# Optimization experiments

Hardware: AMD Instinct MI355X
Metric: run time of the kernel (lower is better)

The kernel has to match this reference:

```python
import jax, jax.numpy as jnp
import numpy as np

B, S, H, NH = 4, 2048, 2048, 16
HD = H // NH  # 128
CAUSAL = True


def setup_inputs() -> dict:
    key = jax.random.key(0)
    ks = jax.random.split(key, 5)
    mk = lambda k: jax.random.normal(k, (H, H), dtype=jnp.float32) * 0.02
    return {
        "x": jax.random.normal(ks[0], (B, S, H), dtype=jnp.float32),
        "w_q": mk(ks[1]),
        "w_k": mk(ks[2]),
        "w_v": mk(ks[3]),
        "w_o": mk(ks[4]),
    }


def reference(x, w_q, w_k, w_v, w_o):
    b, s, _ = x.shape
    # QKV projections (x @ W.T), split into heads: [b, nh, s, hd]
    q = (x @ w_q.T).reshape(b, s, NH, HD).transpose(0, 2, 1, 3)
    k = (x @ w_k.T).reshape(b, s, NH, HD).transpose(0, 2, 1, 3)
    v = (x @ w_v.T).reshape(b, s, NH, HD).transpose(0, 2, 1, 3)
    scale = 1.0 / jnp.sqrt(jnp.asarray(HD, dtype=x.dtype))
    score = jnp.einsum('bhqd,bhkd->bhqk', q, k) * scale  # [b, nh, s, s]
    if CAUSAL:
        mask = jnp.triu(jnp.ones((s, s), dtype=bool), k=1)
        score = jnp.where(mask, -jnp.inf, score)
    attn = jax.nn.softmax(score, axis=-1)
    o = jnp.einsum('bhqk,bhkd->bhqd', attn, v)  # [b, nh, s, hd]
    o = o.transpose(0, 2, 1, 3).reshape(b, s, H)
    return o @ w_o.T
```

## Files before the change

kernel.cpp:

```cpp
#include <hip/hip_runtime.h>

#define S_LEN 2048
#define HSZ   2048
#define M_TOK 8192

typedef float f32x4 __attribute__((ext_vector_type(4)));
typedef __bf16 bf16x8 __attribute__((ext_vector_type(8)));
typedef __bf16 bf16x4 __attribute__((ext_vector_type(4)));

typedef __attribute__((address_space(3))) __bf16 lds_bf16_t;
typedef __attribute__((address_space(1))) const __bf16 glb_bf16_t;

__device__ __forceinline__ void async16(__bf16* ldst, const __bf16* gsrc) {
    __builtin_amdgcn_global_load_lds((glb_bf16_t*)gsrc, (lds_bf16_t*)ldst, 16, 0, 0);
}

#define MFMA16(a, b, c) __builtin_amdgcn_mfma_f32_16x16x32_bf16((a), (b), (c), 0, 0, 0)

__global__ void cast_f32_bf16(const float* __restrict__ s, __bf16* __restrict__ d, int n4) {
    int idx = blockIdx.x * blockDim.x + threadIdx.x;
    int stride = gridDim.x * blockDim.x;
    for (int i = idx; i < n4; i += stride) {
        float4 v = ((const float4*)s)[i];
        bf16x4 o = { (__bf16)v.x, (__bf16)v.y, (__bf16)v.z, (__bf16)v.w };
        ((bf16x4*)d)[i] = o;
    }
}

__global__ void cast_weights(const float* __restrict__ wq, const float* __restrict__ wk,
                             const float* __restrict__ wv, const float* __restrict__ wo,
                             __bf16* __restrict__ wqkvb, __bf16* __restrict__ wob,
                             int n4seg) {
    int idx = blockIdx.x * blockDim.x + threadIdx.x;
    int stride = gridDim.x * blockDim.x;
    int total = 4 * n4seg;
    for (int i = idx; i < total; i += stride) {
        int seg = i / n4seg;
        int off = i - seg * n4seg;
        const float* s = (seg == 0) ? wq : (seg == 1) ? wk : (seg == 2) ? wv : wo;
        __bf16* d = (seg < 3) ? (wqkvb + (size_t)seg * n4seg * 4) : wob;
        float4 v = ((const float4*)s)[off];
        bf16x4 o = { (__bf16)v.x, (__bf16)v.y, (__bf16)v.z, (__bf16)v.w };
        ((bf16x4*)d)[off] = o;
    }
}


#define G_BAR() __builtin_amdgcn_s_barrier()
#define VMC(n)  do { asm volatile("s_waitcnt vmcnt(" #n ")" ::: "memory"); \
                     __builtin_amdgcn_sched_barrier(0); } while (0)

#define STAGE_A(bsel, kofs, half) do { \
    const __bf16* gp_ = A + (size_t)m0 * K + (kofs); \
    __bf16* sp_ = sm + (bsel) * 32768; \
    _Pragma("unroll") \
    for (int i_ = 0; i_ < 2; ++i_) { \
        int g_ = (w * 2 + i_) * 64 + lane; \
        int ri_ = g_ >> 3, c16_ = g_ & 7; \
        int row_ = (half) * 64 + (ri_ & 63) + (ri_ >> 6) * 128; \
        async16(&sp_[row_ * 64 + c16_ * 8], \
                &gp_[(size_t)row_ * K + ((c16_ ^ (row_ & 7)) * 8)]); \
    } } while (0)

#define STAGE_B(bsel, kofs, half) do { \
    const __bf16* gp_ = Bm + (size_t)n0 * K + (kofs); \
    __bf16* sp_ = sm + (bsel) * 32768 + 16384; \
    _Pragma("unroll") \
    for (int i_ = 0; i_ < 2; ++i_) { \
        int g_ = (w * 2 + i_) * 64 + lane; \
        int ri_ = g_ >> 3, c16_ = g_ & 7; \
        int row_ = (half) * 32 + (ri_ & 31) + (ri_ >> 5) * 64; \
        async16(&sp_[row_ * 64 + c16_ * 8], \
                &gp_[(size_t)row_ * K + ((c16_ ^ (row_ & 7)) * 8)]); \
    } } while (0)

#define LOAD_A(bsel, qm) do { \
    const __bf16* ap_ = sm + (bsel) * 32768; \
    _Pragma("unroll") \
    for (int mi_ = 0; mi_ < 4; ++mi_) { \
        int R_ = wm * 128 + (qm) * 64 + mi_ * 16 + l15; \
        int sw_ = (R_ & 7) << 3; \
        af[mi_][0] = *(const bf16x8*)&ap_[R_ * 64 + ((quad * 8) ^ sw_)]; \
        af[mi_][1] = *(const bf16x8*)&ap_[R_ * 64 + ((32 + quad * 8) ^ sw_)]; \
    } } while (0)

#define LOAD_B(bsel, qn, dst) do { \
    const __bf16* bp_ = sm + (bsel) * 32768 + 16384; \
    _Pragma("unroll") \
    for (int ni_ = 0; ni_ < 2; ++ni_) { \
        int R_ = wn * 64 + (qn) * 32 + ni_ * 16 + l15; \
        int sw_ = (R_ & 7) << 3; \
        dst[ni_][0] = *(const bf16x8*)&bp_[R_ * 64 + ((quad * 8) ^ sw_)]; \
        dst[ni_][1] = *(const bf16x8*)&bp_[R_ * 64 + ((32 + quad * 8) ^ sw_)]; \
    } } while (0)

#define MFMA_Q(qm, qn, bsrc) do { \
    __builtin_amdgcn_s_setprio(1); \
    _Pragma("unroll") \
    for (int mi_ = 0; mi_ < 4; ++mi_) \
        _Pragma("unroll") \
        for (int ni_ = 0; ni_ < 2; ++ni_) { \
            acc[(qm) * 4 + mi_][(qn) * 2 + ni_] = \
                MFMA16(af[mi_][0], bsrc[ni_][0], acc[(qm) * 4 + mi_][(qn) * 2 + ni_]); \
            acc[(qm) * 4 + mi_][(qn) * 2 + ni_] = \
                MFMA16(af[mi_][1], bsrc[ni_][1], acc[(qm) * 4 + mi_][(qn) * 2 + ni_]); \
        } \
    __builtin_amdgcn_s_setprio(0); \
} while (0)

#define GEMM256_MAIN() \
    constexpr int K = 2048; \
    const int w = threadIdx.x >> 6, lane = threadIdx.x & 63; \
    const int wm = w >> 2, wn = w & 3; \
    const int quad = lane >> 4, l15 = lane & 15; \
    const int m0 = blockIdx.y * 256, n0 = blockIdx.x * 256; \
    f32x4 acc[8][4] = {}; \
    bf16x8 af[4][2], b0f[2][2], b1f[2][2]; \
    const int NT = K >> 6; \
     \
     \
    STAGE_A(0, 0, 0); STAGE_B(0, 0, 0); STAGE_A(0, 0, 1); STAGE_B(0, 0, 1); \
    VMC(4); \
    G_BAR(); \
    LOAD_A(0, 0); \
    LOAD_B(0, 0, b0f); \
    _Pragma("unroll 2") \
    for (int kt = 0; kt < NT; ++kt) { \
        const int buf = kt & 1, nbuf = buf ^ 1; \
        const int k1 = (kt + 1) << 6; \
         \
        if (kt + 1 < NT) { STAGE_A(nbuf, k1, 0); VMC(2); } else { VMC(0); } \
        G_BAR(); \
        LOAD_B(buf, 1, b1f); \
        MFMA_Q(0, 0, b0f); \
         \
        if (kt + 1 < NT) STAGE_B(nbuf, k1, 0); \
        MFMA_Q(0, 1, b1f); \
        LOAD_A(buf, 1); \
        G_BAR(); \
         \
        if (kt + 1 < NT) { STAGE_A(nbuf, k1, 1); STAGE_B(nbuf, k1, 1); } \
        MFMA_Q(1, 1, b1f); \
        G_BAR(); \
         \
        MFMA_Q(1, 0, b0f); \
        if (kt + 1 < NT) { \
            VMC(4); \
            G_BAR(); \
            LOAD_A(nbuf, 0); \
            LOAD_B(nbuf, 0, b0f); \
        } \
    }

__global__ __launch_bounds__(512, 2) void gemm_qkv8(const __bf16* __restrict__ A,
                                                    const __bf16* __restrict__ Bm,
                                                    __bf16* __restrict__ Qo,
                                                    __bf16* __restrict__ Ko,
                                                    __bf16* __restrict__ VT) {
    __shared__ __bf16 sm[65536];
    GEMM256_MAIN();

    const int seg = n0 >> 11;
    const int nn  = (n0 & 2047) + wn * 64;
    if (seg < 2) {
        __bf16* Cv = seg ? Ko : Qo;
        #pragma unroll
        for (int mi = 0; mi < 8; ++mi)
            #pragma unroll
            for (int ni = 0; ni < 4; ++ni)
                #pragma unroll
                for (int i = 0; i < 4; ++i) {
                    int r = m0 + wm * 128 + mi * 16 + quad * 4 + i;
                    int c = nn + ni * 16 + l15;
                    Cv[(size_t)r * HSZ + c] = (__bf16)acc[mi][ni][i];
                }
    } else {
        #pragma unroll
        for (int mi = 0; mi < 8; ++mi)
            #pragma unroll
            for (int ni = 0; ni < 4; ++ni) {
                int r0 = m0 + wm * 128 + mi * 16 + quad * 4;
                int c  = nn + ni * 16 + l15;
                int bb = r0 >> 11, s = r0 & 2047;
                size_t base = ((size_t)(bb * 2048 + c) << 11) + s;
                bf16x4 v = { (__bf16)acc[mi][ni][0], (__bf16)acc[mi][ni][1],
                             (__bf16)acc[mi][ni][2], (__bf16)acc[mi][ni][3] };
                *(bf16x4*)&VT[base] = v;
            }
    }
}

__global__ __launch_bounds__(512, 2) void gemm_out(const __bf16* __restrict__ A,
                                                   const __bf16* __restrict__ Bm,
                                                   float* __restrict__ C) {
    __shared__ __bf16 sm[65536];
    GEMM256_MAIN();

    #pragma unroll
    for (int mi = 0; mi < 8; ++mi)
        #pragma unroll
        for (int ni = 0; ni < 4; ++ni)
            #pragma unroll
            for (int i = 0; i < 4; ++i) {
                int r = m0 + wm * 128 + mi * 16 + quad * 4 + i;
                int c = n0 + wn * 64 + ni * 16 + l15;
                C[(size_t)r * HSZ + c] = acc[mi][ni][i];
            }
}

__global__ __launch_bounds__(256, 2) void flash_fwd(const __bf16* __restrict__ Q,
                                                    const __bf16* __restrict__ K,
                                                    const __bf16* __restrict__ VT,
                                                    __bf16* __restrict__ O) {
    const int bx = blockIdx.x;
    const int qt = 15 - (bx >> 6);
    const int bh = bx & 63;
    const int q0 = qt * 128;

    const int tid  = threadIdx.x;
    const int w    = tid >> 6;
    const int lane = tid & 63;
    const int quad = lane >> 4;
    const int l15  = lane & 15;

    __shared__ __bf16 Ks[4 * 64 * 32];
    __shared__ __bf16 Vt[2 * 128 * 32];
    __shared__ __bf16 Ps[2 * 128 * 40];

    const int bq = bh >> 4, hh = bh & 15;
    const size_t base = ((size_t)bq * S_LEN) * HSZ + (size_t)hh * 128;
    const __bf16* Qg  = Q + base + (size_t)q0 * HSZ;
    const __bf16* VTg = VT + (size_t)bh * 128 * 2048;

    bf16x8 qf[2][4];
    #pragma unroll
    for (int mb = 0; mb < 2; ++mb)
        #pragma unroll
        for (int ks = 0; ks < 4; ++ks)
            qf[mb][ks] = *(const bf16x8*)&Qg[(size_t)(w * 32 + mb * 16 + l15) * HSZ + ks * 32 + quad * 8];

    f32x4 o_acc[2][8] = {};
    f32x4 psum[2] = {};

    const float scl = 0.08838834764831845f * 1.4426950408889634f;
    const float CC  = 8.0f * 1.4426950408889634f;
    bf16x8 ones;
    #pragma unroll
    for (int j = 0; j < 8; ++j) ones[j] = (__bf16)1.0f;

    const int n_kv = 2 * qt + 2;
    for (int kvt = 0; kvt < n_kv; ++kvt) {
        const int k0r = kvt * 64;
        __syncthreads();

        const __bf16* Kg = K + base + (size_t)k0r * HSZ;
        #pragma unroll
        for (int i = 0; i < 4; ++i) {
            int e  = (w * 4 + i) * 512 + lane * 8;
            int kc = e >> 11, r = (e >> 5) & 63, c = e & 31;
            async16(&Ks[e], &Kg[(size_t)r * HSZ + kc * 32 + c]);
        }
        #pragma unroll
        for (int i = 0; i < 4; ++i) {
            int e   = (w * 4 + i) * 512 + lane * 8;
            int kvc = e >> 12, dd = (e >> 5) & 127, c = e & 31;
            async16(&Vt[e], &VTg[(size_t)dd * 2048 + k0r + kvc * 32 + c]);
        }
        __syncthreads();

        f32x4 s_acc[2][4] = {};
        #pragma unroll
        for (int ks = 0; ks < 4; ++ks)
            #pragma unroll
            for (int nt = 0; nt < 4; ++nt) {
                bf16x8 bk = *(const bf16x8*)&Ks[ks * 2048 + (nt * 16 + l15) * 32 + quad * 8];
                s_acc[0][nt] = MFMA16(qf[0][ks], bk, s_acc[0][nt]);
                s_acc[1][nt] = MFMA16(qf[1][ks], bk, s_acc[1][nt]);
            }

        if (kvt >= 2 * qt) {
            #pragma unroll
            for (int mb = 0; mb < 2; ++mb) {
                int row = q0 + w * 32 + mb * 16 + quad * 4;
                #pragma unroll
                for (int nt = 0; nt < 4; ++nt) {
                    int col = k0r + nt * 16 + l15;
                    #pragma unroll
                    for (int i = 0; i < 4; ++i)
                        if (col > row + i) s_acc[mb][nt][i] = -1e30f;
                }
            }
        }

        #pragma unroll
        for (int mb = 0; mb < 2; ++mb)
            #pragma unroll
            for (int nt = 0; nt < 4; ++nt)
                #pragma unroll
                for (int i = 0; i < 4; ++i) {
                    float p = exp2f(s_acc[mb][nt][i] * scl - CC);
                    Ps[(nt >> 1) * 5120 + (w * 32 + mb * 16 + quad * 4 + i) * 40 + (nt & 1) * 16 + l15] = (__bf16)p;
                }

        #pragma unroll
        for (int ks2 = 0; ks2 < 2; ++ks2) {
            bf16x8 ap0 = *(const bf16x8*)&Ps[ks2 * 5120 + (w * 32 + l15) * 40 + quad * 8];
            bf16x8 ap1 = *(const bf16x8*)&Ps[ks2 * 5120 + (w * 32 + 16 + l15) * 40 + quad * 8];
            psum[0] = MFMA16(ap0, ones, psum[0]);
            psum[1] = MFMA16(ap1, ones, psum[1]);
            #pragma unroll
            for (int nt = 0; nt < 8; ++nt) {
                bf16x8 bv = *(const bf16x8*)&Vt[ks2 * 4096 + (nt * 16 + l15) * 32 + quad * 8];
                o_acc[0][nt] = MFMA16(ap0, bv, o_acc[0][nt]);
                o_acc[1][nt] = MFMA16(ap1, bv, o_acc[1][nt]);
            }
        }
    }

    __bf16* Og = O + base + (size_t)q0 * HSZ;
    #pragma unroll
    for (int mb = 0; mb < 2; ++mb)
        #pragma unroll
        for (int i = 0; i < 4; ++i) {
            float inv = 1.f / psum[mb][i];
            int r = w * 32 + mb * 16 + quad * 4 + i;
            #pragma unroll
            for (int nt = 0; nt < 8; ++nt)
                Og[(size_t)r * HSZ + nt * 16 + l15] = (__bf16)(o_acc[mb][nt][i] * inv);
        }
}

extern "C" void kernel_launch(void* const* d_in, const int* in_sizes, int n_in,
                              void* d_out, int out_size, void* d_ws, size_t ws_size,
                              hipStream_t stream) {
    const float* x  = (const float*)d_in[0];
    const float* wq = (const float*)d_in[1];
    const float* wk = (const float*)d_in[2];
    const float* wv = (const float*)d_in[3];
    const float* wo = (const float*)d_in[4];
    float* out = (float*)d_out;

    const size_t nX = (size_t)M_TOK * HSZ;
    const size_t nW = (size_t)HSZ * HSZ;

    char* ws = (char*)d_ws;
    __bf16* xb    = (__bf16*)ws;  ws += nX * 2;
    __bf16* wqkvb = (__bf16*)ws;  ws += 3 * nW * 2;
    __bf16* wob   = (__bf16*)ws;  ws += nW * 2;
    __bf16* Qb    = (__bf16*)ws;  ws += nX * 2;
    __bf16* Kb    = (__bf16*)ws;  ws += nX * 2;
    __bf16* VTb   = (__bf16*)ws;  ws += nX * 2;
    __bf16* Ob    = (__bf16*)ws;  ws += nX * 2;

    cast_f32_bf16<<<2048, 256, 0, stream>>>(x, xb, (int)(nX / 4));
    cast_weights<<<2048, 256, 0, stream>>>(wq, wk, wv, wo, wqkvb, wob, (int)(nW / 4));

    dim3 gq(3 * HSZ / 256, M_TOK / 256);
    gemm_qkv8<<<gq, 512, 0, stream>>>(xb, wqkvb, Qb, Kb, VTb);

    flash_fwd<<<64 * (S_LEN / 128), 256, 0, stream>>>(Qb, Kb, VTb, Ob);

    dim3 gg(HSZ / 256, M_TOK / 256);
    gemm_out<<<gg, 512, 0, stream>>>(Ob, wob, out);
}
```

Baseline: 509.9 us.

## Double-buffer K/V tiles in flash attention and prefetch the next tile

The flash attention kernel now keeps two LDS buffers for the K and V^T tiles. It issues async global-to-LDS loads for the next KV tile before computing on the current one, so each iteration needs one barrier instead of two and load latency can overlap with MFMA work. The P staging buffer shrinks to one 32-column chunk that is reused across two sub-steps, which offsets the larger K/V footprint. MFMA sections are wrapped in s_setprio raises. Total LDS use grows, which could limit how many blocks fit on a CU.

```diff
diff --git a/kernel.cpp b/kernel.cpp
--- a/kernel.cpp
+++ b/kernel.cpp
@@ -117,8 +117,6 @@
     f32x4 acc[8][4] = {}; \
     bf16x8 af[4][2], b0f[2][2], b1f[2][2]; \
     const int NT = K >> 6; \
-     \
-     \
     STAGE_A(0, 0, 0); STAGE_B(0, 0, 0); STAGE_A(0, 0, 1); STAGE_B(0, 0, 1); \
     VMC(4); \
     G_BAR(); \
@@ -208,6 +206,22 @@
             }
 }
 
+#define FSTAGE(b, kvt_) do { \
+    const int k0s_ = (kvt_) * 64; \
+    const __bf16* Kg_ = K + base + (size_t)k0s_ * HSZ; \
+    _Pragma("unroll") \
+    for (int i_ = 0; i_ < 4; ++i_) { \
+        int e_ = (w * 4 + i_) * 512 + lane * 8; \
+        int kc_ = e_ >> 11, r_ = (e_ >> 5) & 63, c_ = e_ & 31; \
+        async16(&Ks[(b) * 8192 + e_], &Kg_[(size_t)r_ * HSZ + kc_ * 32 + c_]); \
+    } \
+    _Pragma("unroll") \
+    for (int i_ = 0; i_ < 4; ++i_) { \
+        int e_ = (w * 4 + i_) * 512 + lane * 8; \
+        int kvc_ = e_ >> 12, dd_ = (e_ >> 5) & 127, c_ = e_ & 31; \
+        async16(&Vt[(b) * 8192 + e_], &VTg[(size_t)dd_ * 2048 + k0s_ + kvc_ * 32 + c_]); \
+    } } while (0)
+
 __global__ __launch_bounds__(256, 2) void flash_fwd(const __bf16* __restrict__ Q,
                                                     const __bf16* __restrict__ K,
                                                     const __bf16* __restrict__ VT,
@@ -223,9 +237,9 @@
     const int quad = lane >> 4;
     const int l15  = lane & 15;
 
-    __shared__ __bf16 Ks[4 * 64 * 32];
-    __shared__ __bf16 Vt[2 * 128 * 32];
-    __shared__ __bf16 Ps[2 * 128 * 40];
+    __shared__ __bf16 Ks[2 * 4 * 64 * 32];
+    __shared__ __bf16 Vt[2 * 2 * 128 * 32];
+    __shared__ __bf16 Ps[128 * 40];
 
     const int bq = bh >> 4, hh = bh & 15;
     const size_t base = ((size_t)bq * S_LEN) * HSZ + (size_t)hh * 128;
@@ -249,34 +263,27 @@
     for (int j = 0; j < 8; ++j) ones[j] = (__bf16)1.0f;
 
     const int n_kv = 2 * qt + 2;
+
+    FSTAGE(0, 0);
+    __syncthreads();
+
     for (int kvt = 0; kvt < n_kv; ++kvt) {
+        const int b = kvt & 1;
         const int k0r = kvt * 64;
-        __syncthreads();
-
-        const __bf16* Kg = K + base + (size_t)k0r * HSZ;
-        #pragma unroll
-        for (int i = 0; i < 4; ++i) {
-            int e  = (w * 4 + i) * 512 + lane * 8;
-            int kc = e >> 11, r = (e >> 5) & 63, c = e & 31;
-            async16(&Ks[e], &Kg[(size_t)r * HSZ + kc * 32 + c]);
-        }
-        #pragma unroll
-        for (int i = 0; i < 4; ++i) {
-            int e   = (w * 4 + i) * 512 + lane * 8;
-            int kvc = e >> 12, dd = (e >> 5) & 127, c = e & 31;
-            async16(&Vt[e], &VTg[(size_t)dd * 2048 + k0r + kvc * 32 + c]);
-        }
-        __syncthreads();
+
+        if (kvt + 1 < n_kv) FSTAGE(b ^ 1, kvt + 1);
 
         f32x4 s_acc[2][4] = {};
+        __builtin_amdgcn_s_setprio(1);
         #pragma unroll
         for (int ks = 0; ks < 4; ++ks)
             #pragma unroll
             for (int nt = 0; nt < 4; ++nt) {
-                bf16x8 bk = *(const bf16x8*)&Ks[ks * 2048 + (nt * 16 + l15) * 32 + quad * 8];
+                bf16x8 bk = *(const bf16x8*)&Ks[b * 8192 + ks * 2048 + (nt * 16 + l15) * 32 + quad * 8];
                 s_acc[0][nt] = MFMA16(qf[0][ks], bk, s_acc[0][nt]);
                 s_acc[1][nt] = MFMA16(qf[1][ks], bk, s_acc[1][nt]);
             }
+        __builtin_amdgcn_s_setprio(0);
 
         if (kvt >= 2 * qt) {
             #pragma unroll
@@ -293,28 +300,33 @@
         }
 
         #pragma unroll
-        for (int mb = 0; mb < 2; ++mb)
-            #pragma unroll
-            for (int nt = 0; nt < 4; ++nt)
+        for (int ch = 0; ch < 2; ++ch) {
+            #pragma unroll
+            for (int mb = 0; mb < 2; ++mb)
                 #pragma unroll
-                for (int i = 0; i < 4; ++i) {
-                    float p = exp2f(s_acc[mb][nt][i] * scl - CC);
-                    Ps[(nt >> 1) * 5120 + (w * 32 + mb * 16 + quad * 4 + i) * 40 + (nt & 1) * 16 + l15] = (__bf16)p;
+                for (int nt2 = 0; nt2 < 2; ++nt2) {
+                    int nt = ch * 2 + nt2;
+                    #pragma unroll
+                    for (int i = 0; i < 4; ++i) {
+                        float p = exp2f(s_acc[mb][nt][i] * scl - CC);
+                        Ps[(w * 32 + mb * 16 + quad * 4 + i) * 40 + nt2 * 16 + l15] = (__bf16)p;
+                    }
                 }
-
-        #pragma unroll
-        for (int ks2 = 0; ks2 < 2; ++ks2) {
-            bf16x8 ap0 = *(const bf16x8*)&Ps[ks2 * 5120 + (w * 32 + l15) * 40 + quad * 8];
-            bf16x8 ap1 = *(const bf16x8*)&Ps[ks2 * 5120 + (w * 32 + 16 + l15) * 40 + quad * 8];
+            bf16x8 ap0 = *(const bf16x8*)&Ps[(w * 32 + l15) * 40 + quad * 8];
+            bf16x8 ap1 = *(const bf16x8*)&Ps[(w * 32 + 16 + l15) * 40 + quad * 8];
             psum[0] = MFMA16(ap0, ones, psum[0]);
             psum[1] = MFMA16(ap1, ones, psum[1]);
+            __builtin_amdgcn_s_setprio(1);
             #pragma unroll
             for (int nt = 0; nt < 8; ++nt) {
-                bf16x8 bv = *(const bf16x8*)&Vt[ks2 * 4096 + (nt * 16 + l15) * 32 + quad * 8];
+                bf16x8 bv = *(const bf16x8*)&Vt[b * 8192 + ch * 4096 + (nt * 16 + l15) * 32 + quad * 8];
                 o_acc[0][nt] = MFMA16(ap0, bv, o_acc[0][nt]);
                 o_acc[1][nt] = MFMA16(ap1, bv, o_acc[1][nt]);
             }
+            __builtin_amdgcn_s_setprio(0);
         }
+
+        __syncthreads();
     }
 
     __bf16* Og = O + base + (size_t)q0 * HSZ;
```

Measured after the change: 507.0 us. Within noise of the previous version (-0.6%).
